# Kernel optimization log

Measured on AMD Instinct MI355X. Metric: run time of the kernel, lower is better.

Reference implementation:

```python
import jax, jax.numpy as jnp
import numpy as np

VOCAB, HIDDEN = 128, 1024
BATCH, SEQ = 64, 512


def setup_inputs() -> dict:
    key = jax.random.key(0)
    ks = jax.random.split(key, 6)
    scale = 1.0 / np.sqrt(HIDDEN)
    return {
        "x": jax.random.randint(ks[0], (BATCH, SEQ), 0, VOCAB, dtype=jnp.int32),
        "h": jnp.zeros((BATCH, HIDDEN), dtype=jnp.float32),
        "emb": jax.random.normal(ks[1], (VOCAB, HIDDEN), dtype=jnp.float32),
        "W_hx": jax.random.normal(ks[2], (HIDDEN, HIDDEN), dtype=jnp.float32) * scale,
        "b_hx": jnp.zeros((HIDDEN,), dtype=jnp.float32),
        "W_hh": jax.random.normal(ks[3], (HIDDEN, HIDDEN), dtype=jnp.float32) * scale,
        "W_out": jax.random.normal(ks[4], (HIDDEN, VOCAB), dtype=jnp.float32) * scale,
        "b_out": jnp.zeros((VOCAB,), dtype=jnp.float32),
    }


def reference(x, h, emb, W_hx, b_hx, W_hh, W_out, b_out):
    # x: [B, S] int indices; h: [B, H] initial hidden state
    x_emb = emb[x]  # [B, S, H] embedding lookup

    def step(h, xt):  # xt: [B, H]
        h_new = jnp.tanh(xt @ W_hx + b_hx + h @ W_hh)
        return h_new, h_new

    # scan over time axis (sequential dependency on h)
    h_final, hs = jax.lax.scan(step, h, jnp.swapaxes(x_emb, 0, 1))  # hs: [S, B, H]
    out = jnp.swapaxes(hs, 0, 1)  # [B, S, H]
    logits = out @ W_out + b_out  # [B, S, V]
    return logits, h_final
```

## Files before the change

kernel.cpp:

```cpp
#include <hip/hip_runtime.h>
#include <stdint.h>
#include <stddef.h>

#define VOCAB  128
#define HIDDEN 1024
#define BATCH  64
#define SEQ    512

#define NGROUP 4
#define BG     16
#define NWG    32
#define CJ     32
#define NVW    4
#define NTHR   512

#define POISON 0x7F800000u

#define E2_OFF   0
#define WOT_OFF  131072
#define BUF_OFF  196608

typedef __attribute__((ext_vector_type(8))) short short8_t;
typedef __attribute__((ext_vector_type(4))) float f32x4;

__device__ __forceinline__ uint4 cload4u(const void* p) {
    uint4 v;
    asm volatile("global_load_dwordx4 %0, %1, off sc0 sc1" : "=v"(v) : "v"(p));
    return v;
}
__device__ __forceinline__ void cstoreu(unsigned int* p, unsigned int x) {
    asm volatile("global_store_dword %0, %1, off sc0 sc1" :: "v"(p), "v"(x) : "memory");
}
#define WAITVM0() asm volatile("s_waitcnt vmcnt(0)" ::: "memory")
#define SCHED_FENCE() __builtin_amdgcn_sched_barrier(0)

__device__ __forceinline__ unsigned short bf16_rne(float f) {
    unsigned int u = __float_as_uint(f);
    u += 0x7FFF + ((u >> 16) & 1);
    return (unsigned short)(u >> 16);
}
__device__ __forceinline__ float bf16_f32(unsigned short h) {
    return __uint_as_float(((unsigned int)h) << 16);
}
__device__ __forceinline__ bool ok8(const uint4 a, const uint4 b) {
    return a.x != POISON && a.y != POISON && a.z != POISON && a.w != POISON
        && b.x != POISON && b.y != POISON && b.z != POISON && b.w != POISON;
}
__device__ __forceinline__ void unpack8(const uint4 a, const uint4 b,
                                        short8_t* h8, short8_t* l8) {
    (*h8)[0]=(short)(a.x>>16); (*l8)[0]=(short)(a.x&0xFFFF);
    (*h8)[1]=(short)(a.y>>16); (*l8)[1]=(short)(a.y&0xFFFF);
    (*h8)[2]=(short)(a.z>>16); (*l8)[2]=(short)(a.z&0xFFFF);
    (*h8)[3]=(short)(a.w>>16); (*l8)[3]=(short)(a.w&0xFFFF);
    (*h8)[4]=(short)(b.x>>16); (*l8)[4]=(short)(b.x&0xFFFF);
    (*h8)[5]=(short)(b.y>>16); (*l8)[5]=(short)(b.y&0xFFFF);
    (*h8)[6]=(short)(b.z>>16); (*l8)[6]=(short)(b.z&0xFFFF);
    (*h8)[7]=(short)(b.w>>16); (*l8)[7]=(short)(b.w&0xFFFF);
}

__global__ void e2_kernel(const float* __restrict__ emb, const float* __restrict__ W_hx,
                          const float* __restrict__ b_hx, float* __restrict__ E2) {
    int v = blockIdx.x >> 2;
    int j = (blockIdx.x & 3) * 256 + threadIdx.x;
    const float* er = emb + (size_t)v * HIDDEN;
    float acc = 0.f;
#pragma unroll 8
    for (int k = 0; k < HIDDEN; ++k)
        acc += er[k] * W_hx[(size_t)k * HIDDEN + j];
    E2[(size_t)v * HIDDEN + j] = acc + b_hx[j];
}

__global__ void wot_kernel(const float* __restrict__ W_out, unsigned short* __restrict__ WoT) {
    int v  = blockIdx.x;
    int k4 = threadIdx.x;
    ushort4 r;
    r.x = bf16_rne(W_out[(size_t)(k4*4+0)*VOCAB + v]);
    r.y = bf16_rne(W_out[(size_t)(k4*4+1)*VOCAB + v]);
    r.z = bf16_rne(W_out[(size_t)(k4*4+2)*VOCAB + v]);
    r.w = bf16_rne(W_out[(size_t)(k4*4+3)*VOCAB + v]);
    ((ushort4*)(WoT + (size_t)v * HIDDEN))[k4] = r;
}

__global__ void poison_kernel(unsigned int* __restrict__ bufs) {
    int i = blockIdx.x * 256 + threadIdx.x;
    ((uint4*)bufs)[i] = make_uint4(POISON, POISON, POISON, POISON);
}

extern "C" __global__ void __launch_bounds__(NTHR, 2)
rnn_kernel(const int* __restrict__ x, const float* __restrict__ h0,
           const float* __restrict__ W_hh,
           const float* __restrict__ E2, const unsigned short* __restrict__ WoT,
           const float* __restrict__ b_out,
           unsigned int* __restrict__ bufs,
           float* __restrict__ logits, float* __restrict__ hf) {
    extern __shared__ char lds_raw[];
    short* sHi  = (short*)lds_raw;
    float* sPart = (float*)(lds_raw + 32768);
    int*   sX   = (int*)(lds_raw + 49152);

    const int wg = blockIdx.x;
    const int g  = wg / NWG;
    const int w  = wg % NWG;
    const int b0 = g * BG;
    const int j0 = w * CJ;
    const int tid  = threadIdx.x;
    const int lane = tid & 63;
    const int wv   = tid >> 6;
    const int r    = lane & 15;
    const int kg   = lane >> 4;

    {
        const int4* xs4 = (const int4*)(x + (size_t)b0 * SEQ);
#pragma unroll
        for (int i = 0; i < 4; ++i)
            ((int4*)sX)[tid + 512 * i] = xs4[tid + 512 * i];
    }

    short8_t whi[2][4], wlo[2][4];
    {
#pragma unroll
        for (int ct = 0; ct < 2; ++ct) {
            int col = j0 + ct * 16 + r;
#pragma unroll
            for (int c = 0; c < 4; ++c) {
                int kb = wv * 128 + c * 32 + kg * 8;
#pragma unroll
                for (int e = 0; e < 8; ++e) {
                    float wval = W_hh[(size_t)(kb + e) * HIDDEN + col];
                    unsigned short hi = bf16_rne(wval);
                    whi[ct][c][e] = (short)hi;
                    wlo[ct][c][e] = (short)bf16_rne(wval - bf16_f32(hi));
                }
            }
        }
    }

    short8_t wvo[4];
    {
#pragma unroll
        for (int c = 0; c < 4; ++c) {
            int kb = wv * 128 + c * 32 + kg * 8;
#pragma unroll
            for (int e = 0; e < 8; ++e)
                wvo[c][e] = (r < NVW)
                    ? (short)WoT[(size_t)(w * NVW + r) * HIDDEN + kb + e] : (short)0;
        }
    }
    const float boV = (tid < 64) ? b_out[w * NVW + (tid & 3)] : 0.f;
    const int rb = tid >> 5, jb = tid & 31;
    __syncthreads();

    for (int t = 0; t < SEQ; ++t) {
        float e2p = E2[(size_t)sX[rb * SEQ + t] * HIDDEN + j0 + jb];

        short8_t ahi[4], alo[4];
        if (t == 0) {
            const float* hr = h0 + ((size_t)(b0 + r) << 10) + wv * 128 + kg * 8;
#pragma unroll
            for (int c = 0; c < 4; ++c) {
                float4 f0 = *(const float4*)(hr + c * 32);
                float4 f1 = *(const float4*)(hr + c * 32 + 4);
                float fv[8] = {f0.x,f0.y,f0.z,f0.w,f1.x,f1.y,f1.z,f1.w};
#pragma unroll
                for (int e = 0; e < 8; ++e) {
                    unsigned short hi = bf16_rne(fv[e]);
                    ahi[c][e] = (short)hi;
                    alo[c][e] = (short)bf16_rne(fv[e] - bf16_f32(hi));
                }
            }
        } else {
            const unsigned int* src = bufs + ((size_t)((t - 1) & 3) << 16)
                                           + ((size_t)(b0 + r) << 10) + wv * 128 + kg * 8;
            uint4 d0a,d0b,d1a,d1b,d2a,d2b,d3a,d3b;
            unsigned pend = 0xF;
            int guard = 0;
            do {
                if (pend & 1u) { d0a = cload4u(src +  0); d0b = cload4u(src +  4); }
                if (pend & 2u) { d1a = cload4u(src + 32); d1b = cload4u(src + 36); }
                if (pend & 4u) { d2a = cload4u(src + 64); d2b = cload4u(src + 68); }
                if (pend & 8u) { d3a = cload4u(src + 96); d3b = cload4u(src + 100); }
                WAITVM0();
                SCHED_FENCE();
                if ((pend & 1u) && ok8(d0a, d0b)) pend &= ~1u;
                if ((pend & 2u) && ok8(d1a, d1b)) pend &= ~2u;
                if ((pend & 4u) && ok8(d2a, d2b)) pend &= ~4u;
                if ((pend & 8u) && ok8(d3a, d3b)) pend &= ~8u;
                if (!pend) break;
                __builtin_amdgcn_s_sleep(1);
            } while (++guard < (1 << 20));
            SCHED_FENCE();
            unpack8(d0a, d0b, &ahi[0], &alo[0]);
            unpack8(d1a, d1b, &ahi[1], &alo[1]);
            unpack8(d2a, d2b, &ahi[2], &alo[2]);
            unpack8(d3a, d3b, &ahi[3], &alo[3]);
        }

#pragma unroll
        for (int c = 0; c < 4; ++c) {
            int c8 = wv * 16 + c * 4 + kg;
            *(short8_t*)(sHi + r * 1024 + ((c8 ^ (r & 7)) << 3)) = ahi[c];
        }

        f32x4 acc0 = {0.f, 0.f, 0.f, 0.f};
        f32x4 acc1 = {0.f, 0.f, 0.f, 0.f};
#pragma unroll
        for (int c = 0; c < 4; ++c) {
            acc0 = __builtin_amdgcn_mfma_f32_16x16x32_bf16(ahi[c], whi[0][c], acc0, 0, 0, 0);
            acc1 = __builtin_amdgcn_mfma_f32_16x16x32_bf16(ahi[c], whi[1][c], acc1, 0, 0, 0);
            acc0 = __builtin_amdgcn_mfma_f32_16x16x32_bf16(alo[c], whi[0][c], acc0, 0, 0, 0);
            acc1 = __builtin_amdgcn_mfma_f32_16x16x32_bf16(alo[c], whi[1][c], acc1, 0, 0, 0);
            acc0 = __builtin_amdgcn_mfma_f32_16x16x32_bf16(ahi[c], wlo[0][c], acc0, 0, 0, 0);
            acc1 = __builtin_amdgcn_mfma_f32_16x16x32_bf16(ahi[c], wlo[1][c], acc1, 0, 0, 0);
        }
#pragma unroll
        for (int q = 0; q < 4; ++q) {
            sPart[wv * 512 + (kg * 4 + q) * 32 + r]      = acc0[q];
            sPart[wv * 512 + (kg * 4 + q) * 32 + 16 + r] = acc1[q];
        }
        __syncthreads();

        {
            float s = 0.f;
#pragma unroll
            for (int z = 0; z < 8; ++z) s += sPart[z * 512 + tid];
            float hn = tanhf(s + e2p);
            unsigned short hi = bf16_rne(hn);
            unsigned short lo = bf16_rne(hn - bf16_f32(hi));
            unsigned int pk = ((unsigned int)hi << 16) | (unsigned int)lo;
            size_t idx = ((size_t)(b0 + rb) << 10) + j0 + jb;
            cstoreu(bufs + ((size_t)(t & 3) << 16) + idx, pk);
            cstoreu(bufs + ((size_t)((t + 2) & 3) << 16) + idx, POISON);
            if (t == SEQ - 1)
                hf[(size_t)(b0 + rb) * HIDDEN + j0 + jb] = hn;
        }
        __syncthreads();

        if (t > 0) {
            f32x4 accL = {0.f, 0.f, 0.f, 0.f};
#pragma unroll
            for (int c = 0; c < 4; ++c) {
                int c8 = wv * 16 + c * 4 + kg;
                short8_t a8 = *(const short8_t*)(sHi + r * 1024 + ((c8 ^ (r & 7)) << 3));
                accL = __builtin_amdgcn_mfma_f32_16x16x32_bf16(a8, wvo[c], accL, 0, 0, 0);
            }
            if (r < NVW) {
#pragma unroll
                for (int q = 0; q < 4; ++q)
                    sPart[wv * 64 + (kg * 4 + q) * 4 + r] = accL[q];
            }
            __syncthreads();
            if (tid < 64) {
                int b = tid >> 2, v = tid & 3;
                float s = 0.f;
#pragma unroll
                for (int z = 0; z < 8; ++z) s += sPart[z * 64 + b * 4 + v];
                logits[((size_t)(b0 + b) * SEQ + (t - 1)) * VOCAB + w * NVW + v] = s + boV;
            }
        }
    }

    {
        const unsigned int* src = bufs + ((size_t)((SEQ - 1) & 3) << 16)
                                       + ((size_t)(b0 + r) << 10) + wv * 128 + kg * 8;
        uint4 d0a,d0b,d1a,d1b,d2a,d2b,d3a,d3b;
        unsigned pend = 0xF;
        int guard = 0;
        do {
            if (pend & 1u) { d0a = cload4u(src +  0); d0b = cload4u(src +  4); }
            if (pend & 2u) { d1a = cload4u(src + 32); d1b = cload4u(src + 36); }
            if (pend & 4u) { d2a = cload4u(src + 64); d2b = cload4u(src + 68); }
            if (pend & 8u) { d3a = cload4u(src + 96); d3b = cload4u(src + 100); }
            WAITVM0();
            SCHED_FENCE();
            if ((pend & 1u) && ok8(d0a, d0b)) pend &= ~1u;
            if ((pend & 2u) && ok8(d1a, d1b)) pend &= ~2u;
            if ((pend & 4u) && ok8(d2a, d2b)) pend &= ~4u;
            if ((pend & 8u) && ok8(d3a, d3b)) pend &= ~8u;
            if (!pend) break;
            __builtin_amdgcn_s_sleep(1);
        } while (++guard < (1 << 20));
        SCHED_FENCE();
        short8_t h8, l8;
        unpack8(d0a, d0b, &h8, &l8);
        *(short8_t*)(sHi + r * 1024 + (((wv * 16 + 0 * 4 + kg) ^ (r & 7)) << 3)) = h8;
        unpack8(d1a, d1b, &h8, &l8);
        *(short8_t*)(sHi + r * 1024 + (((wv * 16 + 1 * 4 + kg) ^ (r & 7)) << 3)) = h8;
        unpack8(d2a, d2b, &h8, &l8);
        *(short8_t*)(sHi + r * 1024 + (((wv * 16 + 2 * 4 + kg) ^ (r & 7)) << 3)) = h8;
        unpack8(d3a, d3b, &h8, &l8);
        *(short8_t*)(sHi + r * 1024 + (((wv * 16 + 3 * 4 + kg) ^ (r & 7)) << 3)) = h8;
    }
    __syncthreads();
    {
        f32x4 accL = {0.f, 0.f, 0.f, 0.f};
#pragma unroll
        for (int c = 0; c < 4; ++c) {
            int c8 = wv * 16 + c * 4 + kg;
            short8_t a8 = *(const short8_t*)(sHi + r * 1024 + ((c8 ^ (r & 7)) << 3));
            accL = __builtin_amdgcn_mfma_f32_16x16x32_bf16(a8, wvo[c], accL, 0, 0, 0);
        }
        if (r < NVW) {
#pragma unroll
            for (int q = 0; q < 4; ++q)
                sPart[wv * 64 + (kg * 4 + q) * 4 + r] = accL[q];
        }
        __syncthreads();
        if (tid < 64) {
            int b = tid >> 2, v = tid & 3;
            float s = 0.f;
#pragma unroll
            for (int z = 0; z < 8; ++z) s += sPart[z * 64 + b * 4 + v];
            logits[((size_t)(b0 + b) * SEQ + (SEQ - 1)) * VOCAB + w * NVW + v] = s + boV;
        }
    }
}

extern "C" void kernel_launch(void* const* d_in, const int* in_sizes, int n_in,
                              void* d_out, int out_size, void* d_ws, size_t ws_size,
                              hipStream_t stream) {
    (void)in_sizes; (void)n_in; (void)out_size; (void)ws_size;
    const int*   x     = (const int*)  d_in[0];
    const float* h0    = (const float*)d_in[1];
    const float* emb   = (const float*)d_in[2];
    const float* W_hx  = (const float*)d_in[3];
    const float* b_hx  = (const float*)d_in[4];
    const float* W_hh  = (const float*)d_in[5];
    const float* W_out = (const float*)d_in[6];
    const float* b_out = (const float*)d_in[7];

    float* logits = (float*)d_out;
    float* hf     = logits + (size_t)BATCH * SEQ * VOCAB;

    float* ws  = (float*)d_ws;
    float* E2  = ws + E2_OFF;
    unsigned short* WoT = (unsigned short*)(ws + WOT_OFF);
    unsigned int*   bufs = (unsigned int*)(ws + BUF_OFF);

    poison_kernel<<<256, 256, 0, stream>>>(bufs);
    e2_kernel<<<512, 256, 0, stream>>>(emb, W_hx, b_hx, E2);
    wot_kernel<<<128, 256, 0, stream>>>(W_out, WoT);

    hipFuncSetAttribute(reinterpret_cast<const void*>(rnn_kernel),
                        hipFuncAttributeMaxDynamicSharedMemorySize, 81920);
    rnn_kernel<<<NGROUP * NWG, NTHR, 81920, stream>>>(x, h0, W_hh, E2, WoT, b_out,
                                                      bufs, logits, hf);
}
```

Baseline: 1.849 ms.

## Split each workgroup's batch rows into two ping-pong halves to overlap polling

Each workgroup's 16 batch rows are split into two 8-row halves, A and B, processed alternately each timestep. The global-memory poll for one half's hidden state is issued while the other half runs its MFMA recurrence, tanh and logits. Hidden-state loads are restructured into coalesced per-row 16-byte loads, with hi and lo parts staged in separate LDS arrays. The logits reduction is deferred one phase so it overlaps the next half's MFMA work. This aims to hide cross-workgroup synchronization latency, at the cost of using only 8 of the 16 MFMA rows per half and needing more LDS (116 KB).

```diff
diff --git a/kernel.cpp b/kernel.cpp
--- a/kernel.cpp
+++ b/kernel.cpp
@@ -7,8 +7,6 @@
 #define BATCH  64
 #define SEQ    512
 
-#define NGROUP 4
-#define BG     16
 #define NWG    32
 #define CJ     32
 #define NVW    4
@@ -21,6 +19,7 @@
 #define BUF_OFF  196608
 
 typedef __attribute__((ext_vector_type(8))) short short8_t;
+typedef __attribute__((ext_vector_type(4))) short short4_t;
 typedef __attribute__((ext_vector_type(4))) float f32x4;
 
 __device__ __forceinline__ uint4 cload4u(const void* p) {
@@ -42,20 +41,8 @@
 __device__ __forceinline__ float bf16_f32(unsigned short h) {
     return __uint_as_float(((unsigned int)h) << 16);
 }
-__device__ __forceinline__ bool ok8(const uint4 a, const uint4 b) {
-    return a.x != POISON && a.y != POISON && a.z != POISON && a.w != POISON
-        && b.x != POISON && b.y != POISON && b.z != POISON && b.w != POISON;
-}
-__device__ __forceinline__ void unpack8(const uint4 a, const uint4 b,
-                                        short8_t* h8, short8_t* l8) {
-    (*h8)[0]=(short)(a.x>>16); (*l8)[0]=(short)(a.x&0xFFFF);
-    (*h8)[1]=(short)(a.y>>16); (*l8)[1]=(short)(a.y&0xFFFF);
-    (*h8)[2]=(short)(a.z>>16); (*l8)[2]=(short)(a.z&0xFFFF);
-    (*h8)[3]=(short)(a.w>>16); (*l8)[3]=(short)(a.w&0xFFFF);
-    (*h8)[4]=(short)(b.x>>16); (*l8)[4]=(short)(b.x&0xFFFF);
-    (*h8)[5]=(short)(b.y>>16); (*l8)[5]=(short)(b.y&0xFFFF);
-    (*h8)[6]=(short)(b.z>>16); (*l8)[6]=(short)(b.z&0xFFFF);
-    (*h8)[7]=(short)(b.w>>16); (*l8)[7]=(short)(b.w&0xFFFF);
+__device__ __forceinline__ bool ok4(const uint4 v) {
+    return v.x != POISON && v.y != POISON && v.z != POISON && v.w != POISON;
 }
 
 __global__ void e2_kernel(const float* __restrict__ emb, const float* __restrict__ W_hx,
@@ -86,23 +73,89 @@
     ((uint4*)bufs)[i] = make_uint4(POISON, POISON, POISON, POISON);
 }
 
-extern "C" __global__ void __launch_bounds__(NTHR, 2)
+__device__ __forceinline__ void issue4(const unsigned int* src, int lane, uint4* d) {
+#pragma unroll
+    for (int i = 0; i < 4; ++i)
+        d[i] = cload4u(src + i * 256 + lane * 4);
+}
+__device__ __forceinline__ void poll4(const unsigned int* src, int lane, uint4* d) {
+    unsigned pend = 0xF;
+    int guard = 0;
+    for (;;) {
+        WAITVM0();
+        SCHED_FENCE();
+#pragma unroll
+        for (int i = 0; i < 4; ++i)
+            if ((pend >> i) & 1u)
+                if (ok4(d[i])) pend &= ~(1u << i);
+        if (!pend) break;
+        if (++guard > (1 << 20)) break;
+        __builtin_amdgcn_s_sleep(1);
+#pragma unroll
+        for (int i = 0; i < 4; ++i)
+            if ((pend >> i) & 1u)
+                d[i] = cload4u(src + i * 256 + lane * 4);
+    }
+    SCHED_FENCE();
+}
+__device__ __forceinline__ void publish_u32(short* sHi, short* sLo, int row, int lane,
+                                            const uint4* d) {
+#pragma unroll
+    for (int i = 0; i < 4; ++i) {
+        short4_t h4, l4;
+        h4[0]=(short)(d[i].x>>16); l4[0]=(short)(d[i].x&0xFFFF);
+        h4[1]=(short)(d[i].y>>16); l4[1]=(short)(d[i].y&0xFFFF);
+        h4[2]=(short)(d[i].z>>16); l4[2]=(short)(d[i].z&0xFFFF);
+        h4[3]=(short)(d[i].w>>16); l4[3]=(short)(d[i].w&0xFFFF);
+        int c16 = i * 32 + (lane >> 1);
+        int off = row * 1024 + ((c16 ^ row) << 3) + (lane & 1) * 4;
+        *(short4_t*)(sHi + off) = h4;
+        *(short4_t*)(sLo + off) = l4;
+    }
+}
+__device__ __forceinline__ void publish_f32(short* sHi, short* sLo, int row, int lane,
+                                            const float* hr) {
+#pragma unroll
+    for (int i = 0; i < 4; ++i) {
+        float4 f = *(const float4*)(hr + i * 256 + lane * 4);
+        float fv[4] = {f.x, f.y, f.z, f.w};
+        short4_t h4, l4;
+#pragma unroll
+        for (int e = 0; e < 4; ++e) {
+            unsigned short hi = bf16_rne(fv[e]);
+            h4[e] = (short)hi;
+            l4[e] = (short)bf16_rne(fv[e] - bf16_f32(hi));
+        }
+        int c16 = i * 32 + (lane >> 1);
+        int off = row * 1024 + ((c16 ^ row) << 3) + (lane & 1) * 4;
+        *(short4_t*)(sHi + off) = h4;
+        *(short4_t*)(sLo + off) = l4;
+    }
+}
+
+extern "C" __global__ void __launch_bounds__(NTHR)
 rnn_kernel(const int* __restrict__ x, const float* __restrict__ h0,
            const float* __restrict__ W_hh,
            const float* __restrict__ E2, const unsigned short* __restrict__ WoT,
            const float* __restrict__ b_out,
            unsigned int* __restrict__ bufs,
            float* __restrict__ logits, float* __restrict__ hf) {
-    extern __shared__ char lds_raw[];
-    short* sHi  = (short*)lds_raw;
-    float* sPart = (float*)(lds_raw + 32768);
-    int*   sX   = (int*)(lds_raw + 49152);
-
-    const int wg = blockIdx.x;
-    const int g  = wg / NWG;
-    const int w  = wg % NWG;
-    const int b0 = g * BG;
-    const int j0 = w * CJ;
+    extern __shared__ char lds[];
+    short* sHiA  = (short*)(lds);
+    short* sLoA  = (short*)(lds + 16384);
+    short* sHiB  = (short*)(lds + 32768);
+    short* sLoB  = (short*)(lds + 49152);
+    float* sPartA = (float*)(lds + 65536);
+    float* sPartB = (float*)(lds + 73728);
+    float* sPLA   = (float*)(lds + 81920);
+    float* sPLB   = (float*)(lds + 82944);
+    int*   sX     = (int*)(lds + 83968);
+
+    const int bid = blockIdx.x;
+    const int w   = bid & 31;
+    const int p   = bid >> 5;
+    const int b0  = p * 16;
+    const int j0  = w * CJ;
     const int tid  = threadIdx.x;
     const int lane = tid & 63;
     const int wv   = tid >> 6;
@@ -134,7 +187,6 @@
             }
         }
     }
-
     short8_t wvo[4];
     {
 #pragma unroll
@@ -146,173 +198,136 @@
                     ? (short)WoT[(size_t)(w * NVW + r) * HIDDEN + kb + e] : (short)0;
         }
     }
-    const float boV = (tid < 64) ? b_out[w * NVW + (tid & 3)] : 0.f;
-    const int rb = tid >> 5, jb = tid & 31;
+    const float bo = b_out[w * NVW + (tid & 3)];
+    const int rowA = b0 + wv;
+    const int rowB = b0 + 8 + wv;
     __syncthreads();
 
+    uint4 dA[4], dB[4];
+
+#define MFMA_MAIN(SHI, SLO, SPART)                                                   \
+    {                                                                                \
+        f32x4 acc0 = {0.f,0.f,0.f,0.f}, acc1 = {0.f,0.f,0.f,0.f};                    \
+        _Pragma("unroll")                                                            \
+        for (int c = 0; c < 4; ++c) {                                                \
+            int row = r & 7;                                                         \
+            int c8 = wv * 16 + c * 4 + kg;                                           \
+            int off = row * 1024 + ((c8 ^ row) << 3);                                \
+            short8_t ahi = *(const short8_t*)((SHI) + off);                          \
+            short8_t alo = *(const short8_t*)((SLO) + off);                          \
+            acc0 = __builtin_amdgcn_mfma_f32_16x16x32_bf16(ahi, whi[0][c], acc0, 0,0,0); \
+            acc1 = __builtin_amdgcn_mfma_f32_16x16x32_bf16(ahi, whi[1][c], acc1, 0,0,0); \
+            acc0 = __builtin_amdgcn_mfma_f32_16x16x32_bf16(alo, whi[0][c], acc0, 0,0,0); \
+            acc1 = __builtin_amdgcn_mfma_f32_16x16x32_bf16(alo, whi[1][c], acc1, 0,0,0); \
+            acc0 = __builtin_amdgcn_mfma_f32_16x16x32_bf16(ahi, wlo[0][c], acc0, 0,0,0); \
+            acc1 = __builtin_amdgcn_mfma_f32_16x16x32_bf16(ahi, wlo[1][c], acc1, 0,0,0); \
+        }                                                                            \
+        if (kg < 2) {                                                                \
+            _Pragma("unroll")                                                        \
+            for (int q = 0; q < 4; ++q) {                                            \
+                (SPART)[wv * 256 + (kg * 4 + q) * 32 + r]      = acc0[q];            \
+                (SPART)[wv * 256 + (kg * 4 + q) * 32 + 16 + r] = acc1[q];            \
+            }                                                                        \
+        }                                                                            \
+    }
+
+#define MFMA_LOGITS(SHI, SPL)                                                        \
+    {                                                                                \
+        f32x4 L = {0.f,0.f,0.f,0.f};                                                 \
+        _Pragma("unroll")                                                            \
+        for (int c = 0; c < 4; ++c) {                                                \
+            int row = r & 7;                                                         \
+            int c8 = wv * 16 + c * 4 + kg;                                           \
+            short8_t a8 = *(const short8_t*)((SHI) + row * 1024 + ((c8 ^ row) << 3)); \
+            L = __builtin_amdgcn_mfma_f32_16x16x32_bf16(a8, wvo[c], L, 0,0,0);       \
+        }                                                                            \
+        if (kg < 2 && r < NVW) {                                                     \
+            _Pragma("unroll")                                                        \
+            for (int q = 0; q < 4; ++q)                                              \
+                (SPL)[wv * 32 + (kg * 4 + q) * 4 + r] = L[q];                        \
+        }                                                                            \
+    }
+
+#define FINISH(SPART, E2P, GB)                                                       \
+    if (tid < 256) {                                                                 \
+        float s = 0.f;                                                               \
+        _Pragma("unroll")                                                            \
+        for (int z = 0; z < 8; ++z) s += (SPART)[z * 256 + tid];                     \
+        float hn = tanhf(s + (E2P));                                                 \
+        unsigned short hi = bf16_rne(hn);                                            \
+        unsigned short lo = bf16_rne(hn - bf16_f32(hi));                             \
+        unsigned int pk = ((unsigned int)hi << 16) | (unsigned int)lo;               \
+        size_t idx = ((size_t)((GB) + (tid >> 5)) << 10) + j0 + (tid & 31);          \
+        cstoreu(bufs + ((size_t)(t & 3) << 16) + idx, pk);                           \
+        cstoreu(bufs + ((size_t)((t + 2) & 3) << 16) + idx, POISON);                 \
+        if (t == SEQ - 1) hf[idx] = hn;                                              \
+    }
+
+#define LREDUCE(SPL, GB, TP)                                                         \
+    if (tid < 32) {                                                                  \
+        int b = tid >> 2, v = tid & 3;                                               \
+        float s = 0.f;                                                               \
+        _Pragma("unroll")                                                            \
+        for (int z = 0; z < 8; ++z) s += (SPL)[z * 32 + b * 4 + v];                  \
+        logits[((size_t)((GB) + b) * SEQ + (TP)) * VOCAB + w * NVW + v] = s + bo;    \
+    }
+
     for (int t = 0; t < SEQ; ++t) {
-        float e2p = E2[(size_t)sX[rb * SEQ + t] * HIDDEN + j0 + jb];
-
-        short8_t ahi[4], alo[4];
         if (t == 0) {
-            const float* hr = h0 + ((size_t)(b0 + r) << 10) + wv * 128 + kg * 8;
-#pragma unroll
-            for (int c = 0; c < 4; ++c) {
-                float4 f0 = *(const float4*)(hr + c * 32);
-                float4 f1 = *(const float4*)(hr + c * 32 + 4);
-                float fv[8] = {f0.x,f0.y,f0.z,f0.w,f1.x,f1.y,f1.z,f1.w};
-#pragma unroll
-                for (int e = 0; e < 8; ++e) {
-                    unsigned short hi = bf16_rne(fv[e]);
-                    ahi[c][e] = (short)hi;
-                    alo[c][e] = (short)bf16_rne(fv[e] - bf16_f32(hi));
-                }
-            }
+            publish_f32(sHiA, sLoA, wv, lane, h0 + ((size_t)rowA << 10));
         } else {
-            const unsigned int* src = bufs + ((size_t)((t - 1) & 3) << 16)
-                                           + ((size_t)(b0 + r) << 10) + wv * 128 + kg * 8;
-            uint4 d0a,d0b,d1a,d1b,d2a,d2b,d3a,d3b;
-            unsigned pend = 0xF;
-            int guard = 0;
-            do {
-                if (pend & 1u) { d0a = cload4u(src +  0); d0b = cload4u(src +  4); }
-                if (pend & 2u) { d1a = cload4u(src + 32); d1b = cload4u(src + 36); }
-                if (pend & 4u) { d2a = cload4u(src + 64); d2b = cload4u(src + 68); }
-                if (pend & 8u) { d3a = cload4u(src + 96); d3b = cload4u(src + 100); }
-                WAITVM0();
-                SCHED_FENCE();
-                if ((pend & 1u) && ok8(d0a, d0b)) pend &= ~1u;
-                if ((pend & 2u) && ok8(d1a, d1b)) pend &= ~2u;
-                if ((pend & 4u) && ok8(d2a, d2b)) pend &= ~4u;
-                if ((pend & 8u) && ok8(d3a, d3b)) pend &= ~8u;
-                if (!pend) break;
-                __builtin_amdgcn_s_sleep(1);
-            } while (++guard < (1 << 20));
-            SCHED_FENCE();
-            unpack8(d0a, d0b, &ahi[0], &alo[0]);
-            unpack8(d1a, d1b, &ahi[1], &alo[1]);
-            unpack8(d2a, d2b, &ahi[2], &alo[2]);
-            unpack8(d3a, d3b, &ahi[3], &alo[3]);
-        }
-
-#pragma unroll
-        for (int c = 0; c < 4; ++c) {
-            int c8 = wv * 16 + c * 4 + kg;
-            *(short8_t*)(sHi + r * 1024 + ((c8 ^ (r & 7)) << 3)) = ahi[c];
-        }
-
-        f32x4 acc0 = {0.f, 0.f, 0.f, 0.f};
-        f32x4 acc1 = {0.f, 0.f, 0.f, 0.f};
-#pragma unroll
-        for (int c = 0; c < 4; ++c) {
-            acc0 = __builtin_amdgcn_mfma_f32_16x16x32_bf16(ahi[c], whi[0][c], acc0, 0, 0, 0);
-            acc1 = __builtin_amdgcn_mfma_f32_16x16x32_bf16(ahi[c], whi[1][c], acc1, 0, 0, 0);
-            acc0 = __builtin_amdgcn_mfma_f32_16x16x32_bf16(alo[c], whi[0][c], acc0, 0, 0, 0);
-            acc1 = __builtin_amdgcn_mfma_f32_16x16x32_bf16(alo[c], whi[1][c], acc1, 0, 0, 0);
-            acc0 = __builtin_amdgcn_mfma_f32_16x16x32_bf16(ahi[c], wlo[0][c], acc0, 0, 0, 0);
-            acc1 = __builtin_amdgcn_mfma_f32_16x16x32_bf16(ahi[c], wlo[1][c], acc1, 0, 0, 0);
-        }
-#pragma unroll
-        for (int q = 0; q < 4; ++q) {
-            sPart[wv * 512 + (kg * 4 + q) * 32 + r]      = acc0[q];
-            sPart[wv * 512 + (kg * 4 + q) * 32 + 16 + r] = acc1[q];
-        }
+            poll4(bufs + ((size_t)((t - 1) & 3) << 16) + ((size_t)rowA << 10), lane, dA);
+            publish_u32(sHiA, sLoA, wv, lane, dA);
+        }
+        if (t > 0)
+            issue4(bufs + ((size_t)((t - 1) & 3) << 16) + ((size_t)rowB << 10), lane, dB);
+        float e2pA = 0.f;
+        if (tid < 256)
+            e2pA = E2[(size_t)sX[(tid >> 5) * SEQ + t] * HIDDEN + j0 + (tid & 31)];
         __syncthreads();
-
-        {
-            float s = 0.f;
-#pragma unroll
-            for (int z = 0; z < 8; ++z) s += sPart[z * 512 + tid];
-            float hn = tanhf(s + e2p);
-            unsigned short hi = bf16_rne(hn);
-            unsigned short lo = bf16_rne(hn - bf16_f32(hi));
-            unsigned int pk = ((unsigned int)hi << 16) | (unsigned int)lo;
-            size_t idx = ((size_t)(b0 + rb) << 10) + j0 + jb;
-            cstoreu(bufs + ((size_t)(t & 3) << 16) + idx, pk);
-            cstoreu(bufs + ((size_t)((t + 2) & 3) << 16) + idx, POISON);
-            if (t == SEQ - 1)
-                hf[(size_t)(b0 + rb) * HIDDEN + j0 + jb] = hn;
-        }
+        if (t >= 2) LREDUCE(sPLB, b0 + 8, t - 2);
+        MFMA_MAIN(sHiA, sLoA, sPartA);
         __syncthreads();
-
-        if (t > 0) {
-            f32x4 accL = {0.f, 0.f, 0.f, 0.f};
-#pragma unroll
-            for (int c = 0; c < 4; ++c) {
-                int c8 = wv * 16 + c * 4 + kg;
-                short8_t a8 = *(const short8_t*)(sHi + r * 1024 + ((c8 ^ (r & 7)) << 3));
-                accL = __builtin_amdgcn_mfma_f32_16x16x32_bf16(a8, wvo[c], accL, 0, 0, 0);
-            }
-            if (r < NVW) {
-#pragma unroll
-                for (int q = 0; q < 4; ++q)
-                    sPart[wv * 64 + (kg * 4 + q) * 4 + r] = accL[q];
-            }
-            __syncthreads();
-            if (tid < 64) {
-                int b = tid >> 2, v = tid & 3;
-                float s = 0.f;
-#pragma unroll
-                for (int z = 0; z < 8; ++z) s += sPart[z * 64 + b * 4 + v];
-                logits[((size_t)(b0 + b) * SEQ + (t - 1)) * VOCAB + w * NVW + v] = s + boV;
-            }
-        }
-    }
-
+        FINISH(sPartA, e2pA, b0);
+        MFMA_LOGITS(sHiA, sPLA);
+
+        if (t == 0) {
+            publish_f32(sHiB, sLoB, wv, lane, h0 + ((size_t)rowB << 10));
+        } else {
+            poll4(bufs + ((size_t)((t - 1) & 3) << 16) + ((size_t)rowB << 10), lane, dB);
+            publish_u32(sHiB, sLoB, wv, lane, dB);
+        }
+        if (t < SEQ - 1)
+            issue4(bufs + ((size_t)(t & 3) << 16) + ((size_t)rowA << 10), lane, dA);
+        float e2pB = 0.f;
+        if (tid < 256)
+            e2pB = E2[(size_t)sX[(8 + (tid >> 5)) * SEQ + t] * HIDDEN + j0 + (tid & 31)];
+        __syncthreads();
+        if (t >= 1) LREDUCE(sPLA, b0, t - 1);
+        MFMA_MAIN(sHiB, sLoB, sPartB);
+        __syncthreads();
+        FINISH(sPartB, e2pB, b0 + 8);
+        MFMA_LOGITS(sHiB, sPLB);
+    }
+
+    __syncthreads();
+    LREDUCE(sPLB, b0 + 8, SEQ - 2);
     {
-        const unsigned int* src = bufs + ((size_t)((SEQ - 1) & 3) << 16)
-                                       + ((size_t)(b0 + r) << 10) + wv * 128 + kg * 8;
-        uint4 d0a,d0b,d1a,d1b,d2a,d2b,d3a,d3b;
-        unsigned pend = 0xF;
-        int guard = 0;
-        do {
-            if (pend & 1u) { d0a = cload4u(src +  0); d0b = cload4u(src +  4); }
-            if (pend & 2u) { d1a = cload4u(src + 32); d1b = cload4u(src + 36); }
-            if (pend & 4u) { d2a = cload4u(src + 64); d2b = cload4u(src + 68); }
-            if (pend & 8u) { d3a = cload4u(src + 96); d3b = cload4u(src + 100); }
-            WAITVM0();
-            SCHED_FENCE();
-            if ((pend & 1u) && ok8(d0a, d0b)) pend &= ~1u;
-            if ((pend & 2u) && ok8(d1a, d1b)) pend &= ~2u;
-            if ((pend & 4u) && ok8(d2a, d2b)) pend &= ~4u;
-            if ((pend & 8u) && ok8(d3a, d3b)) pend &= ~8u;
-            if (!pend) break;
-            __builtin_amdgcn_s_sleep(1);
-        } while (++guard < (1 << 20));
-        SCHED_FENCE();
-        short8_t h8, l8;
-        unpack8(d0a, d0b, &h8, &l8);
-        *(short8_t*)(sHi + r * 1024 + (((wv * 16 + 0 * 4 + kg) ^ (r & 7)) << 3)) = h8;
-        unpack8(d1a, d1b, &h8, &l8);
-        *(short8_t*)(sHi + r * 1024 + (((wv * 16 + 1 * 4 + kg) ^ (r & 7)) << 3)) = h8;
-        unpack8(d2a, d2b, &h8, &l8);
-        *(short8_t*)(sHi + r * 1024 + (((wv * 16 + 2 * 4 + kg) ^ (r & 7)) << 3)) = h8;
-        unpack8(d3a, d3b, &h8, &l8);
-        *(short8_t*)(sHi + r * 1024 + (((wv * 16 + 3 * 4 + kg) ^ (r & 7)) << 3)) = h8;
+        const unsigned int* sA = bufs + ((size_t)((SEQ - 1) & 3) << 16) + ((size_t)rowA << 10);
+        const unsigned int* sB = bufs + ((size_t)((SEQ - 1) & 3) << 16) + ((size_t)rowB << 10);
+        issue4(sA, lane, dA);
+        poll4(sA, lane, dA);
+        issue4(sB, lane, dB);
+        poll4(sB, lane, dB);
+        publish_u32(sHiA, sLoA, wv, lane, dA);
+        publish_u32(sHiB, sLoB, wv, lane, dB);
     }
     __syncthreads();
-    {
-        f32x4 accL = {0.f, 0.f, 0.f, 0.f};
-#pragma unroll
-        for (int c = 0; c < 4; ++c) {
-            int c8 = wv * 16 + c * 4 + kg;
-            short8_t a8 = *(const short8_t*)(sHi + r * 1024 + ((c8 ^ (r & 7)) << 3));
-            accL = __builtin_amdgcn_mfma_f32_16x16x32_bf16(a8, wvo[c], accL, 0, 0, 0);
-        }
-        if (r < NVW) {
-#pragma unroll
-            for (int q = 0; q < 4; ++q)
-                sPart[wv * 64 + (kg * 4 + q) * 4 + r] = accL[q];
-        }
-        __syncthreads();
-        if (tid < 64) {
-            int b = tid >> 2, v = tid & 3;
-            float s = 0.f;
-#pragma unroll
-            for (int z = 0; z < 8; ++z) s += sPart[z * 64 + b * 4 + v];
-            logits[((size_t)(b0 + b) * SEQ + (SEQ - 1)) * VOCAB + w * NVW + v] = s + boV;
-        }
-    }
+    MFMA_LOGITS(sHiA, sPLA);
+    MFMA_LOGITS(sHiB, sPLB);
+    __syncthreads();
+    LREDUCE(sPLA, b0, SEQ - 1);
+    LREDUCE(sPLB, b0 + 8, SEQ - 1);
 }
 
 extern "C" void kernel_launch(void* const* d_in, const int* in_sizes, int n_in,
@@ -341,7 +356,7 @@
     wot_kernel<<<128, 256, 0, stream>>>(W_out, WoT);
 
     hipFuncSetAttribute(reinterpret_cast<const void*>(rnn_kernel),
-                        hipFuncAttributeMaxDynamicSharedMemorySize, 81920);
-    rnn_kernel<<<NGROUP * NWG, NTHR, 81920, stream>>>(x, h0, W_hh, E2, WoT, b_out,
-                                                      bufs, logits, hf);
-}
+                        hipFuncAttributeMaxDynamicSharedMemorySize, 116736);
+    rnn_kernel<<<128, NTHR, 116736, stream>>>(x, h0, W_hh, E2, WoT, b_out,
+                                              bufs, logits, hf);
+}
```

Result: slower. 2.021 ms (+9.3%).
